# Kernel tuning notes

Hardware: AMD Instinct MI355X
Metric: run time of the kernel (lower is better)

The kernel has to match this reference:

```python
import jax, jax.numpy as jnp
import numpy as np

NUM_NODES = 100000
NUM_EDGES = 3200000
NUM_GRAPHS = 512
IN_DIM, OUT_DIM = 128, 16
DIMS = [IN_DIM, 32, 48, 64]


def glorot(key, shape):
    lim = float(np.sqrt(6.0 / (shape[0] + shape[1])))
    return jax.random.uniform(key, shape, jnp.float32, -lim, lim)


def setup_inputs() -> dict:
    key = jax.random.key(0)
    ks = jax.random.split(key, 12)
    x = jax.random.normal(ks[0], (NUM_NODES, IN_DIM), jnp.float32)
    edge_index = jax.random.randint(ks[1], (2, NUM_EDGES), 0, NUM_NODES, jnp.int64)
    batch = jnp.sort(jax.random.randint(ks[2], (NUM_NODES,), 0, NUM_GRAPHS, jnp.int64))
    params = {}
    for i in range(3):
        params[f"W{i+1}"] = glorot(ks[3 + i], (DIMS[i], DIMS[i + 1]))
        params[f"b{i+1}"] = jnp.zeros((DIMS[i + 1],), jnp.float32)
    params["fc1_w"] = glorot(ks[6], (64, 32))
    params["fc1_b"] = jnp.zeros((32,), jnp.float32)
    params["fc2_w"] = glorot(ks[7], (32, OUT_DIM))
    params["fc2_b"] = jnp.zeros((OUT_DIM,), jnp.float32)
    return {"x": x, "edge_index": edge_index, "batch": batch, **params}


def gcn_conv(x, W, b, src, dst, deg_inv_sqrt):
    # h = x @ W; aggregate with symmetric normalization + self loops (PyG GCNConv)
    h = x @ W  # [N, out]
    norm = deg_inv_sqrt[src] * deg_inv_sqrt[dst]  # [E]
    msg = h[src] * norm[:, None]  # [E, out]  (gather)
    agg = jnp.zeros_like(h).at[dst].add(msg)  # scatter-add to targets
    self_loop = h * (deg_inv_sqrt * deg_inv_sqrt)[:, None]
    return agg + self_loop + b


def reference(x, edge_index, batch, W1, b1, W2, b2, W3, b3, fc1_w, fc1_b, fc2_w, fc2_b):
    src, dst = edge_index[0], edge_index[1]
    n = x.shape[0]
    # degree with self loops: deg[i] = in-degree + 1
    deg = jnp.zeros((n,), jnp.float32).at[dst].add(1.0) + 1.0
    dis = jax.lax.rsqrt(deg)
    h = jax.nn.relu(gcn_conv(x, W1, b1, src, dst, dis))
    h = jax.nn.relu(gcn_conv(h, W2, b2, src, dst, dis))
    h = jax.nn.relu(gcn_conv(h, W3, b3, src, dst, dis))
    # global mean pool per graph
    sums = jax.ops.segment_sum(h, batch, num_segments=NUM_GRAPHS)
    cnts = jax.ops.segment_sum(jnp.ones((n,), jnp.float32), batch, num_segments=NUM_GRAPHS)
    pooled = sums / jnp.maximum(cnts, 1.0)[:, None]  # [G, 64]
    z = jax.nn.relu(pooled @ fc1_w + fc1_b)
    logits = z @ fc2_w + fc2_b
    return jax.nn.softmax(logits, axis=1)
```

## Files before the change

### kernel.cpp

```cpp
#include <hip/hip_runtime.h>
#include <hip/hip_fp16.h>

static constexpr int NN = 100000;
static constexpr int NE = 3200000;
static constexpr int NG = 512;
static constexpr int NCB = 196;
static constexpr int CHK = 8192;
static constexpr int NCH = (NE + CHK - 1) / CHK;
static constexpr int NCNT = NCB * NCH;
static constexpr int SCAN_BLK = 2048;
static constexpr int NSB = (NCNT + SCAN_BLK - 1) / SCAN_BLK;

typedef float f32x2 __attribute__((ext_vector_type(2)));

__device__ __forceinline__ void set2_fp8x4(unsigned v, f32x2* a) {
    a[0] = __builtin_amdgcn_cvt_pk_f32_fp8((int)v, false);
    a[1] = __builtin_amdgcn_cvt_pk_f32_fp8((int)v, true);
}
__device__ __forceinline__ void acc2_fp8x4(unsigned v, f32x2* a) {
    a[0] += __builtin_amdgcn_cvt_pk_f32_fp8((int)v, false);
    a[1] += __builtin_amdgcn_cvt_pk_f32_fp8((int)v, true);
}
__device__ __forceinline__ unsigned pack_fp8x4(float a, float b, float c, float d) {
    int p = __builtin_amdgcn_cvt_pk_fp8_f32(a, b, 0, false);
    p = __builtin_amdgcn_cvt_pk_fp8_f32(c, d, p, true);
    return (unsigned)p;
}
__device__ __forceinline__ unsigned pkh2(float a, float b) {
    __half2 h = __floats2half2_rn(a, b);
    return *(unsigned*)&h;
}

__global__ __launch_bounds__(256) void k_histC(const int4* __restrict__ dst4,
                                               int* __restrict__ cntC, int e4) {
    __shared__ int h[NCB];
    for (int i = threadIdx.x; i < NCB; i += 256) h[i] = 0;
    __syncthreads();
    const int s4 = blockIdx.x * (CHK / 4), e4end = min(s4 + CHK / 4, e4);
    for (int i = s4 + threadIdx.x; i < e4end; i += 256) {
        int4 d = dst4[i];
        atomicAdd(&h[d.x >> 9], 1);
        atomicAdd(&h[d.y >> 9], 1);
        atomicAdd(&h[d.z >> 9], 1);
        atomicAdd(&h[d.w >> 9], 1);
    }
    __syncthreads();
    for (int i = threadIdx.x; i < NCB; i += 256)
        cntC[(size_t)i * NCH + blockIdx.x] = h[i];
}

__global__ __launch_bounds__(256) void k_scanA(const int* __restrict__ in,
                                               int* __restrict__ out,
                                               int* __restrict__ bsum, int n) {
    __shared__ int s[256];
    const int tid = threadIdx.x;
    const int base = blockIdx.x * SCAN_BLK + tid * 8;
    int v[8], t = 0;
#pragma unroll
    for (int c = 0; c < 8; c++) {
        int idx = base + c;
        v[c] = (idx < n) ? in[idx] : 0;
        t += v[c];
    }
    s[tid] = t;
    __syncthreads();
    for (int off = 1; off < 256; off <<= 1) {
        int x = (tid >= off) ? s[tid - off] : 0;
        __syncthreads();
        s[tid] += x;
        __syncthreads();
    }
    if (tid == 255) bsum[blockIdx.x] = s[255];
    int run = s[tid] - t;
#pragma unroll
    for (int c = 0; c < 8; c++) {
        int idx = base + c;
        if (idx < n) out[idx] = run;
        run += v[c];
    }
}

__global__ __launch_bounds__(256) void k_scanB(int* __restrict__ bsum, int nb) {
    __shared__ int s[256];
    const int tid = threadIdx.x;
    int v = (tid < nb) ? bsum[tid] : 0;
    s[tid] = v;
    __syncthreads();
    for (int off = 1; off < 256; off <<= 1) {
        int x = (tid >= off) ? s[tid - off] : 0;
        __syncthreads();
        s[tid] += x;
        __syncthreads();
    }
    if (tid < nb) bsum[tid] = s[tid] - v;
}

__global__ __launch_bounds__(256) void k_scatC(const int4* __restrict__ src4,
                                               const int4* __restrict__ dst4,
                                               const int* __restrict__ sc,
                                               const int* __restrict__ bsum,
                                               unsigned* __restrict__ tmp, int e4) {
    __shared__ int cur[NCB];
    for (int i = threadIdx.x; i < NCB; i += 256) {
        size_t idx = (size_t)i * NCH + blockIdx.x;
        cur[i] = sc[idx] + bsum[idx >> 11];
    }
    __syncthreads();
    const int s4 = blockIdx.x * (CHK / 4), e4end = min(s4 + CHK / 4, e4);
    for (int i = s4 + threadIdx.x; i < e4end; i += 256) {
        int4 d = dst4[i];
        int4 sv = src4[i];
        int p0 = atomicAdd(&cur[d.x >> 9], 1);
        tmp[p0] = ((unsigned)(d.x & 511) << 17) | (unsigned)sv.x;
        int p1 = atomicAdd(&cur[d.y >> 9], 1);
        tmp[p1] = ((unsigned)(d.y & 511) << 17) | (unsigned)sv.y;
        int p2 = atomicAdd(&cur[d.z >> 9], 1);
        tmp[p2] = ((unsigned)(d.z & 511) << 17) | (unsigned)sv.z;
        int p3 = atomicAdd(&cur[d.w >> 9], 1);
        tmp[p3] = ((unsigned)(d.w & 511) << 17) | (unsigned)sv.w;
    }
}

__global__ __launch_bounds__(1024) void k_fill512(const unsigned* __restrict__ tmp,
                                                  const int* __restrict__ sc,
                                                  const int* __restrict__ bsum,
                                                  int* __restrict__ csr,
                                                  int* __restrict__ degi,
                                                  int* __restrict__ offs,
                                                  float* __restrict__ dis,
                                                  int n, int etotal) {
    __shared__ int cnt[512];
    __shared__ int s[512];
    __shared__ int cur[512];
    const int b = blockIdx.x, tid = threadIdx.x;
    if (tid < 512) cnt[tid] = 0;
    size_t i0 = (size_t)b * NCH;
    const int e0 = sc[i0] + bsum[i0 >> 11];
    int e1 = etotal;
    if (b + 1 < NCB) {
        size_t i1 = (size_t)(b + 1) * NCH;
        e1 = sc[i1] + bsum[i1 >> 11];
    }
    __syncthreads();
    for (int e = e0 + tid; e < e1; e += 1024)
        atomicAdd(&cnt[tmp[e] >> 17], 1);
    __syncthreads();
    int v = 0;
    if (tid < 512) { v = cnt[tid]; s[tid] = v; }
    __syncthreads();
    for (int off = 1; off < 512; off <<= 1) {
        int x = 0;
        if (tid < 512 && tid >= off) x = s[tid - off];
        __syncthreads();
        if (tid < 512) s[tid] += x;
        __syncthreads();
    }
    if (tid < 512) {
        int c = e0 + s[tid] - v;
        cur[tid] = c;
        int node = b * 512 + tid;
        if (node < n) {
            degi[node] = v;
            offs[node] = c;
            dis[node] = rsqrtf((float)v + 1.0f);
        }
    }
    __syncthreads();
    for (int e = e0 + tid; e < e1; e += 1024) {
        unsigned pk = tmp[e];
        int p = atomicAdd(&cur[pk >> 17], 1);
        csr[p] = (int)(pk & 0x1FFFFu);
    }
}

__global__ __launch_bounds__(256) void k_gemm1(const float* __restrict__ X,
                                               const float* __restrict__ W,
                                               const float* __restrict__ dis,
                                               unsigned* __restrict__ H, int n) {
    constexpr int IN = 128, ROWS = 32;
    __shared__ float sW[IN * 32];
    __shared__ float sX[ROWS][IN];
    const int tid = threadIdx.x;
    for (int i = tid; i < IN * 32; i += 256) sW[i] = W[i];
    const int row0 = blockIdx.x * ROWS;
    const float4* X4 = (const float4*)X;
    for (int i = tid; i < ROWS * 32; i += 256) {
        int r = row0 + (i >> 5);
        float4 v = make_float4(0.f, 0.f, 0.f, 0.f);
        if (r < n) v = X4[(size_t)r * 32 + (i & 31)];
        ((float4*)&sX[i >> 5][0])[i & 31] = v;
    }
    __syncthreads();
    const int lr = tid >> 3;
    const int cg = tid & 7;
    const int gr = row0 + lr;
    float acc[4] = {0.f, 0.f, 0.f, 0.f};
#pragma unroll 8
    for (int k = 0; k < IN; k++) {
        float xv = sX[lr][k];
#pragma unroll
        for (int c = 0; c < 4; c++)
            acc[c] = fmaf(xv, sW[k * 32 + 4 * cg + c], acc[c]);
    }
    if (gr < n) {
        float dd = dis[gr];
        H[(size_t)gr * 8 + cg] =
            pack_fp8x4(acc[0] * dd, acc[1] * dd, acc[2] * dd, acc[3] * dd);
    }
}

__global__ __launch_bounds__(256) void k_pull2(
        const uint2* __restrict__ Hp, const int* __restrict__ offs,
        const int* __restrict__ degi, const int* __restrict__ csr,
        const float* __restrict__ dis, const float* __restrict__ b,
        uint2* __restrict__ A, int n) {
    const int group = threadIdx.x >> 2, j0 = threadIdx.x & 3;
    const int d = blockIdx.x * 64 + group;
    if (d >= n) return;
    f32x2 acc[4];
    uint2 sv = Hp[(size_t)d * 4 + j0];
    set2_fp8x4(sv.x, acc); set2_fp8x4(sv.y, acc + 2);
    int e = offs[d];
    const int end = e + degi[d];
    for (; e + 7 < end; e += 8) {
        uint2 v0 = Hp[(size_t)csr[e] * 4 + j0];
        uint2 v1 = Hp[(size_t)csr[e + 1] * 4 + j0];
        uint2 v2 = Hp[(size_t)csr[e + 2] * 4 + j0];
        uint2 v3 = Hp[(size_t)csr[e + 3] * 4 + j0];
        uint2 v4 = Hp[(size_t)csr[e + 4] * 4 + j0];
        uint2 v5 = Hp[(size_t)csr[e + 5] * 4 + j0];
        uint2 v6 = Hp[(size_t)csr[e + 6] * 4 + j0];
        uint2 v7 = Hp[(size_t)csr[e + 7] * 4 + j0];
        acc2_fp8x4(v0.x, acc); acc2_fp8x4(v0.y, acc + 2);
        acc2_fp8x4(v1.x, acc); acc2_fp8x4(v1.y, acc + 2);
        acc2_fp8x4(v2.x, acc); acc2_fp8x4(v2.y, acc + 2);
        acc2_fp8x4(v3.x, acc); acc2_fp8x4(v3.y, acc + 2);
        acc2_fp8x4(v4.x, acc); acc2_fp8x4(v4.y, acc + 2);
        acc2_fp8x4(v5.x, acc); acc2_fp8x4(v5.y, acc + 2);
        acc2_fp8x4(v6.x, acc); acc2_fp8x4(v6.y, acc + 2);
        acc2_fp8x4(v7.x, acc); acc2_fp8x4(v7.y, acc + 2);
    }
    for (; e < end; e++) {
        uint2 v = Hp[(size_t)csr[e] * 4 + j0];
        acc2_fp8x4(v.x, acc); acc2_fp8x4(v.y, acc + 2);
    }
    const float dd = dis[d];
    float r[8];
#pragma unroll
    for (int c = 0; c < 4; c++) {
        r[2 * c]     = fmaxf(fmaf(acc[c].x, dd, b[8 * j0 + 2 * c]), 0.f) * dd;
        r[2 * c + 1] = fmaxf(fmaf(acc[c].y, dd, b[8 * j0 + 2 * c + 1]), 0.f) * dd;
    }
    A[(size_t)d * 4 + j0] = make_uint2(pack_fp8x4(r[0], r[1], r[2], r[3]),
                                       pack_fp8x4(r[4], r[5], r[6], r[7]));
}

__global__ __launch_bounds__(256) void k_pullmm32(
        const uint2* __restrict__ Hp, const int* __restrict__ offs,
        const int* __restrict__ degi, const int* __restrict__ csr,
        const float* __restrict__ dis, const float* __restrict__ W,
        const float* __restrict__ b, unsigned* __restrict__ A, int n) {
    __shared__ float sW[32 * 48];
    __shared__ float rows[64][33];
    for (int i = threadIdx.x; i < 32 * 48; i += 256) sW[i] = W[i];
    const int group = threadIdx.x >> 2, j0 = threadIdx.x & 3;
    const int d = blockIdx.x * 64 + group;
    if (d < n) {
        f32x2 acc[4];
        uint2 sv = Hp[(size_t)d * 4 + j0];
        set2_fp8x4(sv.x, acc); set2_fp8x4(sv.y, acc + 2);
        int e = offs[d];
        const int end = e + degi[d];
        for (; e + 7 < end; e += 8) {
            uint2 v0 = Hp[(size_t)csr[e] * 4 + j0];
            uint2 v1 = Hp[(size_t)csr[e + 1] * 4 + j0];
            uint2 v2 = Hp[(size_t)csr[e + 2] * 4 + j0];
            uint2 v3 = Hp[(size_t)csr[e + 3] * 4 + j0];
            uint2 v4 = Hp[(size_t)csr[e + 4] * 4 + j0];
            uint2 v5 = Hp[(size_t)csr[e + 5] * 4 + j0];
            uint2 v6 = Hp[(size_t)csr[e + 6] * 4 + j0];
            uint2 v7 = Hp[(size_t)csr[e + 7] * 4 + j0];
            acc2_fp8x4(v0.x, acc); acc2_fp8x4(v0.y, acc + 2);
            acc2_fp8x4(v1.x, acc); acc2_fp8x4(v1.y, acc + 2);
            acc2_fp8x4(v2.x, acc); acc2_fp8x4(v2.y, acc + 2);
            acc2_fp8x4(v3.x, acc); acc2_fp8x4(v3.y, acc + 2);
            acc2_fp8x4(v4.x, acc); acc2_fp8x4(v4.y, acc + 2);
            acc2_fp8x4(v5.x, acc); acc2_fp8x4(v5.y, acc + 2);
            acc2_fp8x4(v6.x, acc); acc2_fp8x4(v6.y, acc + 2);
            acc2_fp8x4(v7.x, acc); acc2_fp8x4(v7.y, acc + 2);
        }
        for (; e < end; e++) {
            uint2 v = Hp[(size_t)csr[e] * 4 + j0];
            acc2_fp8x4(v.x, acc); acc2_fp8x4(v.y, acc + 2);
        }
        const float dd = dis[d];
#pragma unroll
        for (int c = 0; c < 4; c++) {
            rows[group][8 * j0 + 2 * c]     = acc[c].x * dd;
            rows[group][8 * j0 + 2 * c + 1] = acc[c].y * dd;
        }
    }
    __syncthreads();
    const int row0 = blockIdx.x * 64;
    const int nl = threadIdx.x & 63, cgb = threadIdx.x >> 6;
    const int gr = row0 + nl;
    if (gr < n) {
        const float4* sW4 = (const float4*)sW;
        float s[3][4];
#pragma unroll
        for (int o = 0; o < 3; o++)
#pragma unroll
            for (int c = 0; c < 4; c++) s[o][c] = b[12 * cgb + 4 * o + c];
#pragma unroll 8
        for (int k = 0; k < 32; k++) {
            float rv = rows[nl][k];
#pragma unroll
            for (int o = 0; o < 3; o++) {
                float4 w = sW4[k * 12 + cgb * 3 + o];
                s[o][0] = fmaf(rv, w.x, s[o][0]);
                s[o][1] = fmaf(rv, w.y, s[o][1]);
                s[o][2] = fmaf(rv, w.z, s[o][2]);
                s[o][3] = fmaf(rv, w.w, s[o][3]);
            }
        }
        const float dd2 = dis[gr];
#pragma unroll
        for (int o = 0; o < 3; o++) {
            float r0 = fmaxf(s[o][0], 0.f) * dd2;
            float r1 = fmaxf(s[o][1], 0.f) * dd2;
            float r2 = fmaxf(s[o][2], 0.f) * dd2;
            float r3 = fmaxf(s[o][3], 0.f) * dd2;
            A[(size_t)gr * 16 + cgb * 3 + o] = pack_fp8x4(r0, r1, r2, r3);
        }
        A[(size_t)gr * 16 + 12 + cgb] = 0;
    }
}

__global__ __launch_bounds__(256) void k_pullmm48(
        const uint4* __restrict__ Hp, const int* __restrict__ offs,
        const int* __restrict__ degi, const int* __restrict__ csr,
        const float* __restrict__ dis, const float* __restrict__ W,
        const float* __restrict__ b, __half* __restrict__ A, int n) {
    __shared__ float sW[48 * 64];
    __shared__ float rows[64][49];
    for (int i = threadIdx.x; i < 48 * 64; i += 256) sW[i] = W[i];
    const int group = threadIdx.x >> 2, j0 = threadIdx.x & 3;
    const int d = blockIdx.x * 64 + group;
    if (d < n) {
        f32x2 acc[8];
        uint4 sv = Hp[(size_t)d * 4 + j0];
        set2_fp8x4(sv.x, acc);     set2_fp8x4(sv.y, acc + 2);
        set2_fp8x4(sv.z, acc + 4); set2_fp8x4(sv.w, acc + 6);
        int e = offs[d];
        const int end = e + degi[d];
        for (; e + 3 < end; e += 4) {
            uint4 v0 = Hp[(size_t)csr[e] * 4 + j0];
            uint4 v1 = Hp[(size_t)csr[e + 1] * 4 + j0];
            uint4 v2 = Hp[(size_t)csr[e + 2] * 4 + j0];
            uint4 v3 = Hp[(size_t)csr[e + 3] * 4 + j0];
            acc2_fp8x4(v0.x, acc);     acc2_fp8x4(v0.y, acc + 2);
            acc2_fp8x4(v0.z, acc + 4); acc2_fp8x4(v0.w, acc + 6);
            acc2_fp8x4(v1.x, acc);     acc2_fp8x4(v1.y, acc + 2);
            acc2_fp8x4(v1.z, acc + 4); acc2_fp8x4(v1.w, acc + 6);
            acc2_fp8x4(v2.x, acc);     acc2_fp8x4(v2.y, acc + 2);
            acc2_fp8x4(v2.z, acc + 4); acc2_fp8x4(v2.w, acc + 6);
            acc2_fp8x4(v3.x, acc);     acc2_fp8x4(v3.y, acc + 2);
            acc2_fp8x4(v3.z, acc + 4); acc2_fp8x4(v3.w, acc + 6);
        }
        for (; e < end; e++) {
            uint4 v = Hp[(size_t)csr[e] * 4 + j0];
            acc2_fp8x4(v.x, acc);     acc2_fp8x4(v.y, acc + 2);
            acc2_fp8x4(v.z, acc + 4); acc2_fp8x4(v.w, acc + 6);
        }
        const float dd = dis[d];
        if (j0 < 3) {
#pragma unroll
            for (int c = 0; c < 8; c++) {
                rows[group][16 * j0 + 2 * c]     = acc[c].x * dd;
                rows[group][16 * j0 + 2 * c + 1] = acc[c].y * dd;
            }
        }
    }
    __syncthreads();
    const int row0 = blockIdx.x * 64;
    const int nl = threadIdx.x & 63, cgb = threadIdx.x >> 6;
    const int gr = row0 + nl;
    if (gr < n) {
        const float4* sW4 = (const float4*)sW;
        float s[4][4];
#pragma unroll
        for (int o = 0; o < 4; o++)
#pragma unroll
            for (int c = 0; c < 4; c++) s[o][c] = b[16 * cgb + 4 * o + c];
#pragma unroll 8
        for (int k = 0; k < 48; k++) {
            float rv = rows[nl][k];
#pragma unroll
            for (int o = 0; o < 4; o++) {
                float4 w = sW4[k * 16 + cgb * 4 + o];
                s[o][0] = fmaf(rv, w.x, s[o][0]);
                s[o][1] = fmaf(rv, w.y, s[o][1]);
                s[o][2] = fmaf(rv, w.z, s[o][2]);
                s[o][3] = fmaf(rv, w.w, s[o][3]);
            }
        }
        uint4 q0, q1;
        q0.x = pkh2(s[0][0], s[0][1]); q0.y = pkh2(s[0][2], s[0][3]);
        q0.z = pkh2(s[1][0], s[1][1]); q0.w = pkh2(s[1][2], s[1][3]);
        q1.x = pkh2(s[2][0], s[2][1]); q1.y = pkh2(s[2][2], s[2][3]);
        q1.z = pkh2(s[3][0], s[3][1]); q1.w = pkh2(s[3][2], s[3][3]);
        ((uint4*)A)[(size_t)gr * 8 + cgb * 2]     = q0;
        ((uint4*)A)[(size_t)gr * 8 + cgb * 2 + 1] = q1;
    }
}

__global__ __launch_bounds__(256) void k_poolhead(
        const __half* __restrict__ A3, const int* __restrict__ batch,
        const float* __restrict__ f1w, const float* __restrict__ f1b,
        const float* __restrict__ f2w, const float* __restrict__ f2b,
        float* __restrict__ out, int n, int ngr) {
    const int g = blockIdx.x;
    __shared__ int sb[2];
    if (threadIdx.x < 2) {
        int target = g + threadIdx.x;
        int lo = 0, hi = n;
        while (lo < hi) {
            int mid = (lo + hi) >> 1;
            if (batch[mid] < target) lo = mid + 1; else hi = mid;
        }
        sb[threadIdx.x] = lo;
    }
    __syncthreads();
    const int s = sb[0], e = sb[1];
    const int j = threadIdx.x & 63, rl = threadIdx.x >> 6;
    float sum = 0.f;
    for (int node = s + rl; node < e; node += 4)
        sum += fmaxf(__half2float(A3[(size_t)node * 64 + j]), 0.f);
    __shared__ float red[4][64];
    __shared__ float p[64], z[32], lg[16];
    red[rl][j] = sum;
    __syncthreads();
    if (rl == 0)
        p[j] = (red[0][j] + red[1][j] + red[2][j] + red[3][j]) /
               fmaxf((float)(e - s), 1.f);
    __syncthreads();
    const int t = threadIdx.x;
    if (t < 32) {
        float acc = f1b[t];
        for (int k = 0; k < 64; k++) acc = fmaf(p[k], f1w[k * 32 + t], acc);
        z[t] = fmaxf(acc, 0.f);
    }
    __syncthreads();
    if (t < 16) {
        float acc = f2b[t];
        for (int k = 0; k < 32; k++) acc = fmaf(z[k], f2w[k * 16 + t], acc);
        lg[t] = acc;
    }
    __syncthreads();
    if (t < 16) {
        float m = lg[0];
        for (int i = 1; i < 16; i++) m = fmaxf(m, lg[i]);
        float sden = 0.f;
        for (int i = 0; i < 16; i++) sden += expf(lg[i] - m);
        out[g * 16 + t] = expf(lg[t] - m) / sden;
    }
}

extern "C" void kernel_launch(void* const* d_in, const int* in_sizes, int n_in,
                              void* d_out, int out_size, void* d_ws, size_t ws_size,
                              hipStream_t stream) {
    (void)in_sizes; (void)n_in; (void)out_size; (void)ws_size;
    const float* x     = (const float*)d_in[0];
    const int*   ei    = (const int*)d_in[1];
    const int*   batch = (const int*)d_in[2];
    const float* W1 = (const float*)d_in[3];
    const float* b1 = (const float*)d_in[4];
    const float* W2 = (const float*)d_in[5];  const float* b2 = (const float*)d_in[6];
    const float* W3 = (const float*)d_in[7];  const float* b3 = (const float*)d_in[8];
    const float* f1w = (const float*)d_in[9]; const float* f1b = (const float*)d_in[10];
    const float* f2w = (const float*)d_in[11];const float* f2b = (const float*)d_in[12];
    float* out = (float*)d_out;

    const int* src = ei;
    const int* dst = ei + NE;

    float* ws = (float*)d_ws;
    size_t o = 0;
    float* dis    = ws + o; o += NN;
    int*   degi   = (int*)(ws + o); o += NN;
    int*   offs   = (int*)(ws + o); o += NN;
    int*   cntC   = (int*)(ws + o); o += 76640;
    int*   sc     = (int*)(ws + o); o += 76640;
    int*   bsum   = (int*)(ws + o); o += 48;
    int*   csr    = (int*)(ws + o); o += NE;
    unsigned* TA  = (unsigned*)(ws + o); o += NE;
    unsigned* H1  = (unsigned*)(ws + o); o += NN * 8;
    unsigned* H2  = (unsigned*)(ws + o); o += NN * 8;
    unsigned* H3  = (unsigned*)(ws + o); o += NN * 16;

    unsigned* tmp = (unsigned*)TA;
    __half*   A3  = (__half*)TA;

    k_histC<<<NCH, 256, 0, stream>>>((const int4*)dst, cntC, NE / 4);
    k_scanA<<<NSB, 256, 0, stream>>>(cntC, sc, bsum, NCNT);
    k_scanB<<<1, 256, 0, stream>>>(bsum, NSB);
    k_scatC<<<NCH, 256, 0, stream>>>((const int4*)src, (const int4*)dst,
                                     sc, bsum, tmp, NE / 4);
    k_fill512<<<NCB, 1024, 0, stream>>>(tmp, sc, bsum, csr, degi, offs, dis, NN, NE);

    const int PGRID = (NN + 63) / 64;

    k_gemm1<<<(NN + 31) / 32, 256, 0, stream>>>(x, W1, dis, H1, NN);
    k_pull2<<<PGRID, 256, 0, stream>>>((const uint2*)H1, offs, degi, csr, dis, b1,
                                       (uint2*)H2, NN);

    k_pullmm32<<<PGRID, 256, 0, stream>>>((const uint2*)H2, offs, degi, csr, dis,
                                          W2, b2, H3, NN);

    k_pullmm48<<<PGRID, 256, 0, stream>>>(
        (const uint4*)H3, offs, degi, csr, dis, W3, b3, A3, NN);

    k_poolhead<<<NG, 256, 0, stream>>>(A3, batch, f1w, f1b, f2w, f2b, out, NN, NG);
}
```

Baseline: 349.5 us.

## Pack layer-3 features to 48-byte rows and predicate gather tails

The 48-wide fp8 intermediate is now stored as 12 words per node instead of 16 with zero padding. The third-layer pull gathers only three 16-byte chunks per neighbor, and the fourth thread of each group no longer issues loads. All pull kernels replace the unrolled loop plus scalar tail with a predicated 8-wide loop that clamps indices and zeroes out-of-range lanes. This cuts gather bytes and keeps more loads in flight per thread, at the cost of wasted loads on partial final batches and misaligned 48-byte rows that can straddle cache lines.

```diff
diff --git a/kernel.cpp b/kernel.cpp
--- a/kernel.cpp
+++ b/kernel.cpp
@@ -222,27 +222,20 @@
     set2_fp8x4(sv.x, acc); set2_fp8x4(sv.y, acc + 2);
     int e = offs[d];
     const int end = e + degi[d];
-    for (; e + 7 < end; e += 8) {
-        uint2 v0 = Hp[(size_t)csr[e] * 4 + j0];
-        uint2 v1 = Hp[(size_t)csr[e + 1] * 4 + j0];
-        uint2 v2 = Hp[(size_t)csr[e + 2] * 4 + j0];
-        uint2 v3 = Hp[(size_t)csr[e + 3] * 4 + j0];
-        uint2 v4 = Hp[(size_t)csr[e + 4] * 4 + j0];
-        uint2 v5 = Hp[(size_t)csr[e + 5] * 4 + j0];
-        uint2 v6 = Hp[(size_t)csr[e + 6] * 4 + j0];
-        uint2 v7 = Hp[(size_t)csr[e + 7] * 4 + j0];
-        acc2_fp8x4(v0.x, acc); acc2_fp8x4(v0.y, acc + 2);
-        acc2_fp8x4(v1.x, acc); acc2_fp8x4(v1.y, acc + 2);
-        acc2_fp8x4(v2.x, acc); acc2_fp8x4(v2.y, acc + 2);
-        acc2_fp8x4(v3.x, acc); acc2_fp8x4(v3.y, acc + 2);
-        acc2_fp8x4(v4.x, acc); acc2_fp8x4(v4.y, acc + 2);
-        acc2_fp8x4(v5.x, acc); acc2_fp8x4(v5.y, acc + 2);
-        acc2_fp8x4(v6.x, acc); acc2_fp8x4(v6.y, acc + 2);
-        acc2_fp8x4(v7.x, acc); acc2_fp8x4(v7.y, acc + 2);
-    }
-    for (; e < end; e++) {
-        uint2 v = Hp[(size_t)csr[e] * 4 + j0];
-        acc2_fp8x4(v.x, acc); acc2_fp8x4(v.y, acc + 2);
+    for (; e < end; e += 8) {
+        uint2 v[8];
+#pragma unroll
+        for (int i = 0; i < 8; i++) {
+            int ee = e + i;
+            int idx = csr[min(ee, NE - 1)];
+            uint2 t = Hp[(size_t)idx * 4 + j0];
+            if (ee >= end) { t.x = 0u; t.y = 0u; }
+            v[i] = t;
+        }
+#pragma unroll
+        for (int i = 0; i < 8; i++) {
+            acc2_fp8x4(v[i].x, acc); acc2_fp8x4(v[i].y, acc + 2);
+        }
     }
     const float dd = dis[d];
     float r[8];
@@ -271,27 +264,20 @@
         set2_fp8x4(sv.x, acc); set2_fp8x4(sv.y, acc + 2);
         int e = offs[d];
         const int end = e + degi[d];
-        for (; e + 7 < end; e += 8) {
-            uint2 v0 = Hp[(size_t)csr[e] * 4 + j0];
-            uint2 v1 = Hp[(size_t)csr[e + 1] * 4 + j0];
-            uint2 v2 = Hp[(size_t)csr[e + 2] * 4 + j0];
-            uint2 v3 = Hp[(size_t)csr[e + 3] * 4 + j0];
-            uint2 v4 = Hp[(size_t)csr[e + 4] * 4 + j0];
-            uint2 v5 = Hp[(size_t)csr[e + 5] * 4 + j0];
-            uint2 v6 = Hp[(size_t)csr[e + 6] * 4 + j0];
-            uint2 v7 = Hp[(size_t)csr[e + 7] * 4 + j0];
-            acc2_fp8x4(v0.x, acc); acc2_fp8x4(v0.y, acc + 2);
-            acc2_fp8x4(v1.x, acc); acc2_fp8x4(v1.y, acc + 2);
-            acc2_fp8x4(v2.x, acc); acc2_fp8x4(v2.y, acc + 2);
-            acc2_fp8x4(v3.x, acc); acc2_fp8x4(v3.y, acc + 2);
-            acc2_fp8x4(v4.x, acc); acc2_fp8x4(v4.y, acc + 2);
-            acc2_fp8x4(v5.x, acc); acc2_fp8x4(v5.y, acc + 2);
-            acc2_fp8x4(v6.x, acc); acc2_fp8x4(v6.y, acc + 2);
-            acc2_fp8x4(v7.x, acc); acc2_fp8x4(v7.y, acc + 2);
-        }
-        for (; e < end; e++) {
-            uint2 v = Hp[(size_t)csr[e] * 4 + j0];
-            acc2_fp8x4(v.x, acc); acc2_fp8x4(v.y, acc + 2);
+        for (; e < end; e += 8) {
+            uint2 v[8];
+#pragma unroll
+            for (int i = 0; i < 8; i++) {
+                int ee = e + i;
+                int idx = csr[min(ee, NE - 1)];
+                uint2 t = Hp[(size_t)idx * 4 + j0];
+                if (ee >= end) { t.x = 0u; t.y = 0u; }
+                v[i] = t;
+            }
+#pragma unroll
+            for (int i = 0; i < 8; i++) {
+                acc2_fp8x4(v[i].x, acc); acc2_fp8x4(v[i].y, acc + 2);
+            }
         }
         const float dd = dis[d];
 #pragma unroll
@@ -330,14 +316,14 @@
             float r1 = fmaxf(s[o][1], 0.f) * dd2;
             float r2 = fmaxf(s[o][2], 0.f) * dd2;
             float r3 = fmaxf(s[o][3], 0.f) * dd2;
-            A[(size_t)gr * 16 + cgb * 3 + o] = pack_fp8x4(r0, r1, r2, r3);
-        }
-        A[(size_t)gr * 16 + 12 + cgb] = 0;
+            A[(size_t)gr * 12 + cgb * 3 + o] = pack_fp8x4(r0, r1, r2, r3);
+        }
     }
 }
 
 __global__ __launch_bounds__(256) void k_pullmm48(
-        const uint4* __restrict__ Hp, const int* __restrict__ offs,
+        const uint4* __restrict__ Hp,
+        const int* __restrict__ offs,
         const int* __restrict__ degi, const int* __restrict__ csr,
         const float* __restrict__ dis, const float* __restrict__ W,
         const float* __restrict__ b, __half* __restrict__ A, int n) {
@@ -346,39 +332,34 @@
     for (int i = threadIdx.x; i < 48 * 64; i += 256) sW[i] = W[i];
     const int group = threadIdx.x >> 2, j0 = threadIdx.x & 3;
     const int d = blockIdx.x * 64 + group;
-    if (d < n) {
+    if (d < n && j0 < 3) {
         f32x2 acc[8];
-        uint4 sv = Hp[(size_t)d * 4 + j0];
+        uint4 sv = Hp[(size_t)d * 3 + j0];
         set2_fp8x4(sv.x, acc);     set2_fp8x4(sv.y, acc + 2);
         set2_fp8x4(sv.z, acc + 4); set2_fp8x4(sv.w, acc + 6);
         int e = offs[d];
         const int end = e + degi[d];
-        for (; e + 3 < end; e += 4) {
-            uint4 v0 = Hp[(size_t)csr[e] * 4 + j0];
-            uint4 v1 = Hp[(size_t)csr[e + 1] * 4 + j0];
-            uint4 v2 = Hp[(size_t)csr[e + 2] * 4 + j0];
-            uint4 v3 = Hp[(size_t)csr[e + 3] * 4 + j0];
-            acc2_fp8x4(v0.x, acc);     acc2_fp8x4(v0.y, acc + 2);
-            acc2_fp8x4(v0.z, acc + 4); acc2_fp8x4(v0.w, acc + 6);
-            acc2_fp8x4(v1.x, acc);     acc2_fp8x4(v1.y, acc + 2);
-            acc2_fp8x4(v1.z, acc + 4); acc2_fp8x4(v1.w, acc + 6);
-            acc2_fp8x4(v2.x, acc);     acc2_fp8x4(v2.y, acc + 2);
-            acc2_fp8x4(v2.z, acc + 4); acc2_fp8x4(v2.w, acc + 6);
-            acc2_fp8x4(v3.x, acc);     acc2_fp8x4(v3.y, acc + 2);
-            acc2_fp8x4(v3.z, acc + 4); acc2_fp8x4(v3.w, acc + 6);
-        }
-        for (; e < end; e++) {
-            uint4 v = Hp[(size_t)csr[e] * 4 + j0];
-            acc2_fp8x4(v.x, acc);     acc2_fp8x4(v.y, acc + 2);
-            acc2_fp8x4(v.z, acc + 4); acc2_fp8x4(v.w, acc + 6);
+        for (; e < end; e += 8) {
+            uint4 v[8];
+#pragma unroll
+            for (int i = 0; i < 8; i++) {
+                int ee = e + i;
+                int idx = csr[min(ee, NE - 1)];
+                uint4 t = Hp[(size_t)idx * 3 + j0];
+                if (ee >= end) { t.x = 0u; t.y = 0u; t.z = 0u; t.w = 0u; }
+                v[i] = t;
+            }
+#pragma unroll
+            for (int i = 0; i < 8; i++) {
+                acc2_fp8x4(v[i].x, acc);     acc2_fp8x4(v[i].y, acc + 2);
+                acc2_fp8x4(v[i].z, acc + 4); acc2_fp8x4(v[i].w, acc + 6);
+            }
         }
         const float dd = dis[d];
-        if (j0 < 3) {
-#pragma unroll
-            for (int c = 0; c < 8; c++) {
-                rows[group][16 * j0 + 2 * c]     = acc[c].x * dd;
-                rows[group][16 * j0 + 2 * c + 1] = acc[c].y * dd;
-            }
+#pragma unroll
+        for (int c = 0; c < 8; c++) {
+            rows[group][16 * j0 + 2 * c]     = acc[c].x * dd;
+            rows[group][16 * j0 + 2 * c + 1] = acc[c].y * dd;
         }
     }
     __syncthreads();
@@ -496,7 +477,7 @@
     unsigned* TA  = (unsigned*)(ws + o); o += NE;
     unsigned* H1  = (unsigned*)(ws + o); o += NN * 8;
     unsigned* H2  = (unsigned*)(ws + o); o += NN * 8;
-    unsigned* H3  = (unsigned*)(ws + o); o += NN * 16;
+    unsigned* H3  = (unsigned*)(ws + o); o += NN * 12;
 
     unsigned* tmp = (unsigned*)TA;
     __half*   A3  = (__half*)TA;
```

Result: faster. 336.3 us (-3.8%).
